# Performance work log

Measured on AMD Instinct MI355X. Metric: run time of the kernel, lower is better.

The kernel has to match this reference:

```python
import jax, jax.numpy as jnp
import numpy as np

NUM_CLASSES = 512  # P distinct identities in the batch (labels are in [0, P))
TAU = 0.5
EPS = 1e-12


def _l2norm(x):
    # F.normalize(x, dim=1) with eps clamp
    n = jnp.sqrt(jnp.sum(x * x, axis=1, keepdims=True))
    return x / jnp.maximum(n, EPS)


def setup_inputs() -> dict:
    key = jax.random.key(0)
    k1, k2, k3 = jax.random.split(key, 3)
    N, D, P = 8192, 2048, NUM_CLASSES
    feat_vp = jax.random.normal(k1, (N, D), dtype=jnp.float32)
    feat_ap = jax.random.normal(k2, (N, D), dtype=jnp.float32)
    feat_rp = jax.random.normal(k3, (N, D), dtype=jnp.float32)
    # P identities, K = N/P instances each; every class present
    label = (jnp.arange(N) % P).astype(jnp.int32)
    return {"feat_vp": feat_vp, "feat_ap": feat_ap, "feat_rp": feat_rp, "label": label}


def reference(feat_vp, feat_ap, feat_rp, label):
    P = NUM_CLASSES
    fv = _l2norm(feat_vp)
    fa = _l2norm(feat_ap)
    fr = _l2norm(feat_rp)

    # segment-mean over labels (replaces the O(N^2 D) python loop)
    counts = jax.ops.segment_sum(jnp.ones_like(label, dtype=fv.dtype), label,
                                 num_segments=P)  # [P]
    inv_cnt = 1.0 / counts[:, None]

    def centers(f):
        s = jax.ops.segment_sum(f, label, num_segments=P)  # [P, D]
        return _l2norm(s * inv_cnt)

    cv, ca, cr = centers(fv), centers(fa), centers(fr)

    # per-sample centers = unique centers gathered back by label
    loss_intra = (jnp.sum((fv - cv[label]) ** 2, axis=1).mean()
                  + jnp.sum((fa - ca[label]) ** 2, axis=1).mean()
                  + jnp.sum((fr - cr[label]) ** 2, axis=1).mean())

    def pair_loss(c1, c2):
        logits = (c1 @ c2.T) / TAU  # [P, P]
        logp = jax.nn.log_softmax(logits, axis=1)
        return -jnp.mean(jnp.diagonal(logp))

    loss_inter = pair_loss(cv, ca) + pair_loss(cv, cr) + pair_loss(ca, cr)
    return loss_intra + loss_inter
```

## Files before the change

kernel.cpp:

```cpp
#include <hip/hip_runtime.h>
#include <hip/hip_bf16.h>

#define P_CLS 512
#define D_DIM 2048
#define CAP   32
#define TAU_INV 2.0f

typedef short short8 __attribute__((ext_vector_type(8)));
typedef float f32x4 __attribute__((ext_vector_type(4)));

__device__ __forceinline__ unsigned short f2bf_bits(float x) {
  __hip_bfloat16 b = __float2bfloat16(x);
  unsigned short u;
  __builtin_memcpy(&u, &b, sizeof(u));
  return u;
}

__device__ __forceinline__ float xred_sum(float v) {
#pragma unroll
  for (int o = 1; o < 64; o <<= 1) v += __shfl_xor(v, o, 64);
  return v;
}
__device__ __forceinline__ float xred_max(float v) {
#pragma unroll
  for (int o = 1; o < 64; o <<= 1) v = fmaxf(v, __shfl_xor(v, o, 64));
  return v;
}

__global__ void k_init(int* cnt, float* accs) {
  int t = blockIdx.x * blockDim.x + threadIdx.x;
  if (t < P_CLS) cnt[t] = 0;
  if (t < 8) accs[t] = 0.f;
}

__global__ void k_index(const int* __restrict__ label, int* __restrict__ cnt,
                        int* __restrict__ idx, int n) {
  int i = blockIdx.x * blockDim.x + threadIdx.x;
  if (i < n) {
    int p = label[i];
    int slot = atomicAdd(&cnt[p], 1);
    if (slot < CAP) idx[p * CAP + slot] = i;
  }
}

__global__ __launch_bounds__(128)
void k_centers(const float* __restrict__ f0, const float* __restrict__ f1,
               const float* __restrict__ f2, const int* __restrict__ cnt,
               const int* __restrict__ idx, __hip_bfloat16* __restrict__ cb,
               float* __restrict__ accs) {
  int wv = threadIdx.x >> 6, lane = threadIdx.x & 63;
  int p = blockIdx.x * 2 + wv;
  int m = blockIdx.y;
  const float* F = (m == 0) ? f0 : (m == 1) ? f1 : f2;
  int c = cnt[p];
  if (c > CAP) c = CAP;
  const int* idxp = idx + p * CAP;
  __hip_bfloat16* dst = cb + ((long)m * P_CLS + p) * D_DIM;

  f32x4 acc[8] = {};
  if (c > 0) {
    f32x4 v[8], nv[8];
    const f32x4* rp = (const f32x4*)(F + (long)idxp[0] * D_DIM);
#pragma unroll
    for (int k = 0; k < 8; ++k) v[k] = rp[lane + k * 64];
    for (int r = 0; r < c; ++r) {
      if (r + 1 < c) {
        const f32x4* np = (const f32x4*)(F + (long)idxp[r + 1] * D_DIM);
#pragma unroll
        for (int k = 0; k < 8; ++k) nv[k] = np[lane + k * 64];
      }
      float ssq = 0.f;
#pragma unroll
      for (int k = 0; k < 8; ++k) {
        f32x4 q = v[k] * v[k];
        ssq += q.x + q.y + q.z + q.w;
      }
      ssq = xred_sum(ssq);
      float w = 1.0f / fmaxf(sqrtf(ssq), 1e-12f);
#pragma unroll
      for (int k = 0; k < 8; ++k) acc[k] += v[k] * w;
#pragma unroll
      for (int k = 0; k < 8; ++k) v[k] = nv[k];
    }
  }
  float s2 = 0.f;
#pragma unroll
  for (int k = 0; k < 8; ++k) {
    f32x4 q = acc[k] * acc[k];
    s2 += q.x + q.y + q.z + q.w;
  }
  s2 = xred_sum(s2);
  float sn = sqrtf(s2);
  float inv = 1.0f / fmaxf(sn, 1e-12f);
#pragma unroll
  for (int k = 0; k < 8; ++k) {
    f32x4 o = acc[k] * inv;
    ushort4 h;
    h.x = f2bf_bits(o.x);
    h.y = f2bf_bits(o.y);
    h.z = f2bf_bits(o.z);
    h.w = f2bf_bits(o.w);
    ((ushort4*)dst)[lane + k * 64] = h;
  }
  if (lane == 0 && c > 0) atomicAdd(&accs[0], sn);
}

__global__ __launch_bounds__(256)
void k_gemm(const __hip_bfloat16* __restrict__ cbh, float* __restrict__ logits) {
  __shared__ __align__(16) unsigned short As[2][64 * 40], Bs[2][64 * 40];
  int pair = blockIdx.y, kz = blockIdx.z;
  int ma = (pair == 2) ? 1 : 0;
  int mb = (pair == 0) ? 1 : 2;
  const unsigned short* A =
      (const unsigned short*)cbh + (long)ma * P_CLS * D_DIM + kz * (D_DIM / 2);
  const unsigned short* B =
      (const unsigned short*)cbh + (long)mb * P_CLS * D_DIM + kz * (D_DIM / 2);
  float* C = logits + ((long)kz * 3 + pair) * P_CLS * P_CLS;
  int tm = (blockIdx.x >> 3) * 64, tn = (blockIdx.x & 7) * 64;
  int t = threadIdx.x, lane = t & 63, wv = t >> 6;
  int srow = t >> 2, skc = (t & 3) * 8;
  int quad = lane >> 4, mr = lane & 15;
  const unsigned short* pa = A + (long)(tm + srow) * D_DIM + skc;
  const unsigned short* pb = B + (long)(tn + srow) * D_DIM + skc;
  f32x4 acc[4] = {{0,0,0,0},{0,0,0,0},{0,0,0,0},{0,0,0,0}};
  uint4 av = *(const uint4*)pa, bv = *(const uint4*)pb;
  *(uint4*)(&As[0][srow * 40 + skc]) = av;
  *(uint4*)(&Bs[0][srow * 40 + skc]) = bv;
  av = *(const uint4*)(pa + 32); bv = *(const uint4*)(pb + 32);
  const int NIT = (D_DIM / 2) / 32;
  for (int it = 0; it < NIT; ++it) {
    __syncthreads();
    int cur = it & 1;
    if (it + 1 < NIT) {
      *(uint4*)(&As[cur ^ 1][srow * 40 + skc]) = av;
      *(uint4*)(&Bs[cur ^ 1][srow * 40 + skc]) = bv;
    }
    if (it + 2 < NIT) {
      av = *(const uint4*)(pa + (it + 2) * 32);
      bv = *(const uint4*)(pb + (it + 2) * 32);
    }
    short8 af = *(const short8*)(&As[cur][(wv * 16 + mr) * 40 + quad * 8]);
#pragma unroll
    for (int nb = 0; nb < 4; ++nb) {
      short8 bfr = *(const short8*)(&Bs[cur][(nb * 16 + mr) * 40 + quad * 8]);
      acc[nb] = __builtin_amdgcn_mfma_f32_16x16x32_bf16(af, bfr, acc[nb], 0, 0, 0);
    }
  }
  int crow = tm + wv * 16 + quad * 4;
#pragma unroll
  for (int nb = 0; nb < 4; ++nb)
#pragma unroll
    for (int r = 0; r < 4; ++r)
      C[(long)(crow + r) * P_CLS + tn + nb * 16 + mr] = acc[nb][r] * TAU_INV;
}

__global__ __launch_bounds__(256)
void k_lse(const float* __restrict__ logits, float* __restrict__ accs) {
  __shared__ float sred[8];
  int row = blockIdx.x;
  int p = row & (P_CLS - 1);
  const float* L0 = logits + (long)row * P_CLS;
  const float* L1 = L0 + 3l * P_CLS * P_CLS;
  int t = threadIdx.x, lane = t & 63, wv = t >> 6;
  float v0 = L0[t] + L1[t];
  float v1 = L0[t + 256] + L1[t + 256];
  float mx = xred_max(fmaxf(v0, v1));
  if (lane == 0) sred[wv] = mx;
  __syncthreads();
  mx = fmaxf(fmaxf(sred[0], sred[1]), fmaxf(sred[2], sred[3]));
  float e = expf(v0 - mx) + expf(v1 - mx);
  e = xred_sum(e);
  if (lane == 0) sred[4 + wv] = e;
  __syncthreads();
  if (t == 0) {
    float tot = sred[4] + sred[5] + sred[6] + sred[7];
    float diag = L0[p] + L1[p];
    atomicAdd(&accs[1], mx + logf(tot) - diag);
  }
}

__global__ void k_final(const float* __restrict__ accs, float* __restrict__ out,
                        float invN) {
  out[0] = 6.0f - 2.0f * invN * accs[0] + accs[1] * (1.0f / (float)P_CLS);
}

extern "C" void kernel_launch(void* const* d_in, const int* in_sizes, int n_in,
                              void* d_out, int out_size, void* d_ws, size_t ws_size,
                              hipStream_t stream) {
  const float* fvp = (const float*)d_in[0];
  const float* fap = (const float*)d_in[1];
  const float* frp = (const float*)d_in[2];
  const int* label = (const int*)d_in[3];
  int N = in_sizes[3];

  char* ws = (char*)d_ws;
  int* cnt = (int*)ws;
  int* idx = (int*)(ws + 2048);
  float* accs = (float*)(ws + 2048 + 65536);
  __hip_bfloat16* cb = (__hip_bfloat16*)(ws + 131072);
  float* logits = (float*)(ws + 131072 + 3ul * P_CLS * D_DIM * 2);

  hipLaunchKernelGGL(k_init, dim3(1), dim3(512), 0, stream, cnt, accs);
  hipLaunchKernelGGL(k_index, dim3((N + 255) / 256), dim3(256), 0, stream,
                     label, cnt, idx, N);
  hipLaunchKernelGGL(k_centers, dim3(P_CLS / 2, 3), dim3(128), 0, stream,
                     fvp, fap, frp, cnt, idx, cb, accs);
  hipLaunchKernelGGL(k_gemm, dim3(64, 3, 2), dim3(256), 0, stream, cb, logits);
  hipLaunchKernelGGL(k_lse, dim3(3 * P_CLS), dim3(256), 0, stream, logits, accs);
  hipLaunchKernelGGL(k_final, dim3(1), dim3(1), 0, stream, accs, (float*)d_out,
                     1.0f / (float)N);
}
```

Measured before the change: 249.0 us.

## Stage center rows through LDS with async loads and raise GEMM split-K

The centers kernel now uses one 256-thread block per class. Batches of 8 member rows are loaded into LDS with global_load_lds async copies, row norms are computed per wave, and the weighted sum is accumulated by all threads. This is meant to give more memory-level parallelism than the old per-wave serial row loop that prefetched only one row ahead. The GEMM split-K factor goes from 2 to 4 when the workspace is large enough, which gives more blocks at the cost of extra partial-logit traffic that k_lse now sums over a variable count.

```diff
diff --git a/kernel.cpp b/kernel.cpp
--- a/kernel.cpp
+++ b/kernel.cpp
@@ -14,6 +14,12 @@
   unsigned short u;
   __builtin_memcpy(&u, &b, sizeof(u));
   return u;
+}
+
+__device__ __forceinline__ void async16(const void* g, void* l) {
+  __builtin_amdgcn_global_load_lds(
+      (const __attribute__((address_space(1))) void*)g,
+      (__attribute__((address_space(3))) void*)l, 16, 0, 0);
 }
 
 __device__ __forceinline__ float xred_sum(float v) {
@@ -43,78 +49,91 @@
   }
 }
 
-__global__ __launch_bounds__(128)
+__global__ __launch_bounds__(256)
 void k_centers(const float* __restrict__ f0, const float* __restrict__ f1,
                const float* __restrict__ f2, const int* __restrict__ cnt,
                const int* __restrict__ idx, __hip_bfloat16* __restrict__ cb,
                float* __restrict__ accs) {
-  int wv = threadIdx.x >> 6, lane = threadIdx.x & 63;
-  int p = blockIdx.x * 2 + wv;
-  int m = blockIdx.y;
+  __shared__ __align__(16) float rows[8 * D_DIM];
+  __shared__ float scr[16];
+  int p = blockIdx.x, m = blockIdx.y;
   const float* F = (m == 0) ? f0 : (m == 1) ? f1 : f2;
+  int t = threadIdx.x, lane = t & 63, wv = t >> 6;
   int c = cnt[p];
   if (c > CAP) c = CAP;
   const int* idxp = idx + p * CAP;
-  __hip_bfloat16* dst = cb + ((long)m * P_CLS + p) * D_DIM;
-
-  f32x4 acc[8] = {};
-  if (c > 0) {
-    f32x4 v[8], nv[8];
-    const f32x4* rp = (const f32x4*)(F + (long)idxp[0] * D_DIM);
-#pragma unroll
-    for (int k = 0; k < 8; ++k) v[k] = rp[lane + k * 64];
-    for (int r = 0; r < c; ++r) {
-      if (r + 1 < c) {
-        const f32x4* np = (const f32x4*)(F + (long)idxp[r + 1] * D_DIM);
-#pragma unroll
-        for (int k = 0; k < 8; ++k) nv[k] = np[lane + k * 64];
+
+  f32x4 acc0 = {0, 0, 0, 0}, acc1 = {0, 0, 0, 0};
+  for (int base = 0; base < c; base += 8) {
+#pragma unroll
+    for (int s = 0; s < 2; ++s) {
+      int rr = 2 * wv + s, gr = base + rr;
+      if (gr < c) {
+        const char* rowp = (const char*)(F + (long)idxp[gr] * D_DIM);
+        char* ldsp = (char*)(rows + rr * D_DIM);
+#pragma unroll
+        for (int j = 0; j < 8; ++j)
+          async16(rowp + j * 1024 + lane * 16, ldsp + j * 1024 + lane * 16);
       }
+    }
+    __syncthreads();
+#pragma unroll
+    for (int s = 0; s < 2; ++s) {
+      int rr = 2 * wv + s;
+      const f32x4* rp = (const f32x4*)(rows + rr * D_DIM);
       float ssq = 0.f;
 #pragma unroll
-      for (int k = 0; k < 8; ++k) {
-        f32x4 q = v[k] * v[k];
+      for (int j = 0; j < 8; ++j) {
+        f32x4 q = rp[lane + 64 * j];
+        q = q * q;
         ssq += q.x + q.y + q.z + q.w;
       }
       ssq = xred_sum(ssq);
-      float w = 1.0f / fmaxf(sqrtf(ssq), 1e-12f);
-#pragma unroll
-      for (int k = 0; k < 8; ++k) acc[k] += v[k] * w;
-#pragma unroll
-      for (int k = 0; k < 8; ++k) v[k] = nv[k];
-    }
-  }
-  float s2 = 0.f;
-#pragma unroll
-  for (int k = 0; k < 8; ++k) {
-    f32x4 q = acc[k] * acc[k];
-    s2 += q.x + q.y + q.z + q.w;
-  }
+      if (lane == 0)
+        scr[rr] = (base + rr < c) ? (1.0f / fmaxf(sqrtf(ssq), 1e-12f)) : 0.f;
+    }
+    __syncthreads();
+#pragma unroll
+    for (int rr = 0; rr < 8; ++rr) {
+      float w = scr[rr];
+      f32x4 x0 = *(const f32x4*)(rows + rr * D_DIM + t * 4);
+      f32x4 x1 = *(const f32x4*)(rows + rr * D_DIM + 1024 + t * 4);
+      acc0 += x0 * w;
+      acc1 += x1 * w;
+    }
+    __syncthreads();
+  }
+  f32x4 q0 = acc0 * acc0, q1 = acc1 * acc1;
+  float s2 = q0.x + q0.y + q0.z + q0.w + q1.x + q1.y + q1.z + q1.w;
   s2 = xred_sum(s2);
+  if (lane == 0) scr[8 + wv] = s2;
+  __syncthreads();
+  s2 = scr[8] + scr[9] + scr[10] + scr[11];
   float sn = sqrtf(s2);
   float inv = 1.0f / fmaxf(sn, 1e-12f);
-#pragma unroll
-  for (int k = 0; k < 8; ++k) {
-    f32x4 o = acc[k] * inv;
-    ushort4 h;
-    h.x = f2bf_bits(o.x);
-    h.y = f2bf_bits(o.y);
-    h.z = f2bf_bits(o.z);
-    h.w = f2bf_bits(o.w);
-    ((ushort4*)dst)[lane + k * 64] = h;
-  }
-  if (lane == 0 && c > 0) atomicAdd(&accs[0], sn);
+  __hip_bfloat16* dst = cb + ((long)m * P_CLS + p) * D_DIM;
+  f32x4 o0 = acc0 * inv, o1 = acc1 * inv;
+  ushort4 h0, h1;
+  h0.x = f2bf_bits(o0.x); h0.y = f2bf_bits(o0.y);
+  h0.z = f2bf_bits(o0.z); h0.w = f2bf_bits(o0.w);
+  h1.x = f2bf_bits(o1.x); h1.y = f2bf_bits(o1.y);
+  h1.z = f2bf_bits(o1.z); h1.w = f2bf_bits(o1.w);
+  ((ushort4*)dst)[t] = h0;
+  ((ushort4*)dst)[t + 256] = h1;
+  if (t == 0 && c > 0) atomicAdd(&accs[0], sn);
 }
 
 __global__ __launch_bounds__(256)
 void k_gemm(const __hip_bfloat16* __restrict__ cbh, float* __restrict__ logits) {
   __shared__ __align__(16) unsigned short As[2][64 * 40], Bs[2][64 * 40];
-  int pair = blockIdx.y, kz = blockIdx.z;
+  int pair = blockIdx.y, kz = blockIdx.z, nkz = gridDim.z;
+  int ksl = D_DIM / nkz;
   int ma = (pair == 2) ? 1 : 0;
   int mb = (pair == 0) ? 1 : 2;
   const unsigned short* A =
-      (const unsigned short*)cbh + (long)ma * P_CLS * D_DIM + kz * (D_DIM / 2);
+      (const unsigned short*)cbh + (long)ma * P_CLS * D_DIM + kz * ksl;
   const unsigned short* B =
-      (const unsigned short*)cbh + (long)mb * P_CLS * D_DIM + kz * (D_DIM / 2);
+      (const unsigned short*)cbh + (long)mb * P_CLS * D_DIM + kz * ksl;
   float* C = logits + ((long)kz * 3 + pair) * P_CLS * P_CLS;
   int tm = (blockIdx.x >> 3) * 64, tn = (blockIdx.x & 7) * 64;
   int t = threadIdx.x, lane = t & 63, wv = t >> 6;
@@ -127,7 +146,7 @@
   *(uint4*)(&As[0][srow * 40 + skc]) = av;
   *(uint4*)(&Bs[0][srow * 40 + skc]) = bv;
   av = *(const uint4*)(pa + 32); bv = *(const uint4*)(pb + 32);
-  const int NIT = (D_DIM / 2) / 32;
+  const int NIT = ksl / 32;
   for (int it = 0; it < NIT; ++it) {
     __syncthreads();
     int cur = it & 1;
@@ -155,15 +174,17 @@
 }
 
 __global__ __launch_bounds__(256)
-void k_lse(const float* __restrict__ logits, float* __restrict__ accs) {
+void k_lse(const float* __restrict__ logits, float* __restrict__ accs, int nkz) {
   __shared__ float sred[8];
   int row = blockIdx.x;
   int p = row & (P_CLS - 1);
-  const float* L0 = logits + (long)row * P_CLS;
-  const float* L1 = L0 + 3l * P_CLS * P_CLS;
   int t = threadIdx.x, lane = t & 63, wv = t >> 6;
-  float v0 = L0[t] + L1[t];
-  float v1 = L0[t + 256] + L1[t + 256];
+  float v0 = 0.f, v1 = 0.f, diag = 0.f;
+  for (int z = 0; z < nkz; ++z) {
+    const float* L = logits + ((long)z * 3 * P_CLS + row) * P_CLS;
+    v0 += L[t];
+    v1 += L[t + 256];
+  }
   float mx = xred_max(fmaxf(v0, v1));
   if (lane == 0) sred[wv] = mx;
   __syncthreads();
@@ -174,7 +195,8 @@
   __syncthreads();
   if (t == 0) {
     float tot = sred[4] + sred[5] + sred[6] + sred[7];
-    float diag = L0[p] + L1[p];
+    for (int z = 0; z < nkz; ++z)
+      diag += logits[((long)z * 3 * P_CLS + row) * P_CLS + p];
     atomicAdd(&accs[1], mx + logf(tot) - diag);
   }
 }
@@ -200,13 +222,17 @@
   __hip_bfloat16* cb = (__hip_bfloat16*)(ws + 131072);
   float* logits = (float*)(ws + 131072 + 3ul * P_CLS * D_DIM * 2);
 
+  size_t base = 131072 + 3ul * P_CLS * D_DIM * 2;
+  size_t per_z = 3ul * P_CLS * P_CLS * 4;
+  int KZ = (ws_size >= base + 4 * per_z) ? 4 : 2;
+
   hipLaunchKernelGGL(k_init, dim3(1), dim3(512), 0, stream, cnt, accs);
   hipLaunchKernelGGL(k_index, dim3((N + 255) / 256), dim3(256), 0, stream,
                      label, cnt, idx, N);
-  hipLaunchKernelGGL(k_centers, dim3(P_CLS / 2, 3), dim3(128), 0, stream,
+  hipLaunchKernelGGL(k_centers, dim3(P_CLS, 3), dim3(256), 0, stream,
                      fvp, fap, frp, cnt, idx, cb, accs);
-  hipLaunchKernelGGL(k_gemm, dim3(64, 3, 2), dim3(256), 0, stream, cb, logits);
-  hipLaunchKernelGGL(k_lse, dim3(3 * P_CLS), dim3(256), 0, stream, logits, accs);
+  hipLaunchKernelGGL(k_gemm, dim3(64, 3, KZ), dim3(256), 0, stream, cb, logits);
+  hipLaunchKernelGGL(k_lse, dim3(3 * P_CLS), dim3(256), 0, stream, logits, accs, KZ);
   hipLaunchKernelGGL(k_final, dim3(1), dim3(1), 0, stream, accs, (float*)d_out,
                      1.0f / (float)N);
 }
```

Measured after the change: 239.7 us. -3.7%, faster.
